# Optimization experiments

Hardware: AMD Instinct MI355X
Metric: run time of the kernel (lower is better)

The kernel has to match this reference:

```python
import jax, jax.numpy as jnp
import numpy as np

VOCAB = 50257
HIDDEN = 1024
CUTOFFS = [0, 20000, 40000, VOCAB]
N_CLUSTERS = 3
N_TOKENS = 4096


def setup_inputs() -> dict:
    key = jax.random.key(0)
    k1, k2, k3, k4 = jax.random.split(key, 4)
    x = jax.random.normal(k1, (N_TOKENS, HIDDEN), dtype=jnp.float32)
    y = jax.random.randint(k2, (N_TOKENS,), 0, VOCAB, dtype=jnp.int64)
    # nn.Linear(hidden, n_clusters, bias=False) weight: [n_clusters, hidden], init std=0.02
    W_cluster = jax.random.normal(k3, (N_CLUSTERS, HIDDEN), dtype=jnp.float32) * 0.02
    logits = jax.random.normal(k4, (HIDDEN, VOCAB), dtype=jnp.float32) * 0.02
    return {"x": x, "y": y, "W_cluster": W_cluster, "logits": logits}


def reference(x, y, W_cluster, logits):
    # cluster head: [N, n_clusters]
    cluster_ll = jax.nn.log_softmax(x @ W_cluster.T, axis=1)
    nll = jnp.zeros(y.shape, dtype=x.dtype)
    for i in range(N_CLUSTERS):  # small fixed loop over clusters
        l, r = CUTOFFS[i], CUTOFFS[i + 1]
        mask = (y >= l) & (y < r)
        # tail logits for this cluster's vocab slice: [N, r-l]
        tail_logprob = jax.nn.log_softmax(x @ logits[:, l:r], axis=1)
        t = jnp.clip(y - l, 0, r - l - 1)  # in-range for masked-out tokens
        tgt_lp = jnp.take_along_axis(tail_logprob, t[:, None], axis=1)[:, 0]
        val = -cluster_ll[:, i] - tgt_lp
        nll = jnp.where(mask, val, nll)
    return nll
```

## Files before the change

kernel.cpp:

```cpp
#include <hip/hip_runtime.h>
#include <math.h>

typedef unsigned short ushort_t;
typedef __attribute__((ext_vector_type(8))) short short8;
typedef __attribute__((ext_vector_type(4))) float floatx4;

constexpr int NT = 4096;
constexpr int H  = 1024;
constexpr int V  = 50257;
constexpr int CUT1 = 20000;
constexpr int CUT2 = 40000;

constexpr int NPAD_TOK = 4352;
constexpr int NPAD_COL = 50560;
constexpr int CT0 = 79, CT1 = 79, CT2 = 41;
constexpr int CT_TOTAL = CT0 + CT1 + CT2;
constexpr int MAX_TTILES = 16;
constexpr int CT_GROUPS = (CT_TOTAL + 7) / 8;
constexpr int MFMA_GRID = 8 * CT_GROUPS * MAX_TTILES;
constexpr int NKT = H / 32;

constexpr int FB_TILES0 = (20000 + 63) / 64;
constexpr int FB_TILES1 = (20000 + 63) / 64;
constexpr int FB_TILES2 = (V - 40000 + 63) / 64;
constexpr int FB_TOTAL = FB_TILES0 + FB_TILES1 + FB_TILES2;

__device__ __forceinline__ ushort_t f2bf(float f) {
  unsigned int u = __float_as_uint(f);
  u = (u + 0x7FFFu + ((u >> 16) & 1u)) >> 16;
  return (ushort_t)u;
}
__device__ __forceinline__ float bf2f(ushort_t b) {
  return __uint_as_float(((unsigned int)b) << 16);
}
__device__ __forceinline__ void gl_lds16(const void* g, void* l) {
  __builtin_amdgcn_global_load_lds(
      (const __attribute__((address_space(1))) void*)g,
      (__attribute__((address_space(3))) void*)l, 16, 0, 0);
}

__global__ __launch_bounds__(1024) void setup_kernel(
    const int* __restrict__ y, int* __restrict__ offsets,
    int* __restrict__ perm, float* __restrict__ sumexp) {
  __shared__ int wcnt[16][3];
  __shared__ int wstart[16][3];
  int tid = threadIdx.x, lane = tid & 63, wid = tid >> 6;
  for (int i = tid; i < NT; i += 1024) sumexp[i] = 0.f;

  int kc[4];
  unsigned long long msk[4][3];
  int cw0 = 0, cw1 = 0, cw2 = 0;
  #pragma unroll
  for (int e = 0; e < 4; e++) {
    int v = y[tid + e * 1024];
    kc[e] = (v >= CUT1) + (v >= CUT2);
    msk[e][0] = __ballot(kc[e] == 0);
    msk[e][1] = __ballot(kc[e] == 1);
    msk[e][2] = __ballot(kc[e] == 2);
    cw0 += __popcll(msk[e][0]);
    cw1 += __popcll(msk[e][1]);
    cw2 += __popcll(msk[e][2]);
  }
  if (lane == 0) { wcnt[wid][0] = cw0; wcnt[wid][1] = cw1; wcnt[wid][2] = cw2; }
  __syncthreads();
  if (tid == 0) {
    int t0 = 0, t1 = 0, t2 = 0;
    for (int wv = 0; wv < 16; wv++) { t0 += wcnt[wv][0]; t1 += wcnt[wv][1]; t2 += wcnt[wv][2]; }
    offsets[0] = 0; offsets[1] = t0; offsets[2] = t0 + t1; offsets[3] = NT;
    int c0 = 0, c1 = t0, c2 = t0 + t1;
    for (int wv = 0; wv < 16; wv++) {
      wstart[wv][0] = c0; c0 += wcnt[wv][0];
      wstart[wv][1] = c1; c1 += wcnt[wv][1];
      wstart[wv][2] = c2; c2 += wcnt[wv][2];
    }
  }
  __syncthreads();
  int r0 = wstart[wid][0], r1 = wstart[wid][1], r2 = wstart[wid][2];
  unsigned long long below = (1ull << lane) - 1ull;
  #pragma unroll
  for (int e = 0; e < 4; e++) {
    int t = tid + e * 1024;
    int c = kc[e];
    int start = (c == 0) ? r0 : ((c == 1) ? r1 : r2);
    perm[start + __popcll(msk[e][c] & below)] = t;
    r0 += __popcll(msk[e][0]);
    r1 += __popcll(msk[e][1]);
    r2 += __popcll(msk[e][2]);
  }
}

__global__ __launch_bounds__(256) void gather_kernel(
    const float* __restrict__ x, const int* __restrict__ perm,
    ushort_t* __restrict__ xb) {
  int p = blockIdx.x;
  int src = (p < NT) ? perm[p] : -1;
  int k = threadIdx.x * 4;
  ushort4 o;
  if (src >= 0) {
    float4 v = *(const float4*)&x[(size_t)src * H + k];
    o.x = f2bf(v.x); o.y = f2bf(v.y); o.z = f2bf(v.z); o.w = f2bf(v.w);
  } else {
    o.x = 0; o.y = 0; o.z = 0; o.w = 0;
  }
  *(ushort4*)&xb[(size_t)p * H + k] = o;
}

__global__ __launch_bounds__(256) void transpose_kernel(
    const float* __restrict__ logits, ushort_t* __restrict__ lt) {
  __shared__ float ts[64][129];
  int col0 = blockIdx.x * 128, k0 = blockIdx.y * 64;
  int tid = threadIdx.x;
  #pragma unroll
  for (int e = 0; e < 8; e++) {
    int i = e * 256 + tid;
    int r = i >> 5, q = i & 31;
    int col = col0 + q * 4;
    float4 v;
    if (col + 3 < V) {
      v = *(const float4*)&logits[(size_t)(k0 + r) * V + col];
    } else {
      v.x = (col + 0 < V) ? logits[(size_t)(k0 + r) * V + col + 0] : 0.f;
      v.y = (col + 1 < V) ? logits[(size_t)(k0 + r) * V + col + 1] : 0.f;
      v.z = (col + 2 < V) ? logits[(size_t)(k0 + r) * V + col + 2] : 0.f;
      v.w = (col + 3 < V) ? logits[(size_t)(k0 + r) * V + col + 3] : 0.f;
    }
    ts[r][4 * q + 0] = v.x;
    ts[r][4 * q + 1] = v.y;
    ts[r][4 * q + 2] = v.z;
    ts[r][4 * q + 3] = v.w;
  }
  __syncthreads();
  #pragma unroll
  for (int e = 0; e < 4; e++) {
    int i = e * 256 + tid;
    int col = i >> 3, kq8 = i & 7;
    short8 o;
    #pragma unroll
    for (int d = 0; d < 8; d++) o[d] = (short)f2bf(ts[8 * kq8 + d][col]);
    *(short8*)&lt[(size_t)(col0 + col) * H + k0 + 8 * kq8] = o;
  }
}

__global__ __launch_bounds__(256) void head_kernel(
    const float* __restrict__ x, const int* __restrict__ y,
    const float* __restrict__ Wc, const ushort_t* __restrict__ lt,
    float* __restrict__ neg_cll, float* __restrict__ z_tgt) {
  int tid = threadIdx.x;
  int lane = tid & 63;
  int token = blockIdx.x * 4 + (tid >> 6);
  int yv = y[token];
  const float* xp = x + (size_t)token * H;
  const ushort_t* lp = lt + (size_t)yv * H;
  float c0 = 0.f, c1 = 0.f, c2 = 0.f, zt = 0.f;
  #pragma unroll
  for (int j = 0; j < 16; j++) {
    int h = lane + j * 64;
    float xv = xp[h];
    c0 = fmaf(xv, Wc[h], c0);
    c1 = fmaf(xv, Wc[H + h], c1);
    c2 = fmaf(xv, Wc[2 * H + h], c2);
    zt = fmaf(xv, bf2f(lp[h]), zt);
  }
  #pragma unroll
  for (int d = 32; d; d >>= 1) {
    c0 += __shfl_down(c0, d);
    c1 += __shfl_down(c1, d);
    c2 += __shfl_down(c2, d);
    zt += __shfl_down(zt, d);
  }
  if (lane == 0) {
    float m = fmaxf(c0, fmaxf(c1, c2));
    float lse = m + logf(expf(c0 - m) + expf(c1 - m) + expf(c2 - m));
    int k = (yv >= CUT1) + (yv >= CUT2);
    float ck = (k == 0) ? c0 : ((k == 1) ? c1 : c2);
    neg_cll[token] = lse - ck;
    z_tgt[token] = zt;
  }
}

__global__ __launch_bounds__(512, 2) void mfma_kernel(
    const ushort_t* __restrict__ xb, const ushort_t* __restrict__ lt,
    const int* __restrict__ offsets, float* __restrict__ sumexp) {
  int id = blockIdx.x;
  int xcd = id & 7;
  int j = id >> 3;
  int ct = xcd + 8 * (j >> 4);
  int tt = j & 15;
  if (ct >= CT_TOTAL) return;

  int c, col0, colEnd;
  if (ct < CT0)            { c = 0; col0 = ct * 256;                      colEnd = CUT1; }
  else if (ct < CT0 + CT1) { c = 1; col0 = CUT1 + (ct - CT0) * 256;       colEnd = CUT2; }
  else                     { c = 2; col0 = CUT2 + (ct - CT0 - CT1) * 256; colEnd = V; }

  int t0 = offsets[c] + tt * 256;
  int tEnd = offsets[c + 1];
  if (t0 >= tEnd) return;

  __shared__ __align__(16) ushort_t As[4][128 * 64];
  __shared__ __align__(16) ushort_t Bs[4][128 * 64];

  int tid = threadIdx.x;
  int lane = tid & 63;
  int w = tid >> 6;
  int wm = w >> 2, wn = w & 3;
  int m_in = lane & 15, quad = lane >> 4;

  const ushort_t* gA[2];
  const ushort_t* gB[2];
  #pragma unroll
  for (int cc = 0; cc < 2; cc++) {
    int lr = w * 16 + cc * 8 + (lane >> 3);
    int ls = lane & 7;
    int m  = 2 * lr + (ls >> 2);
    int q  = (ls & 3) ^ (lr & 3);
    gA[cc] = xb + (size_t)(t0 + m) * H + q * 8;
    gB[cc] = lt + (size_t)(col0 + m) * H + q * 8;
  }
  int ks = 0;
  auto STAGE = [&]() {
    int b = ks & 3;
    #pragma unroll
    for (int cc = 0; cc < 2; cc++) {
      gl_lds16(gA[cc], &As[b][(w * 16 + cc * 8) * 64]);
      gl_lds16(gB[cc], &Bs[b][(w * 16 + cc * 8) * 64]);
      gA[cc] += 32; gB[cc] += 32;
    }
    ++ks;
  };

  int sxor = quad ^ ((m_in >> 1) & 3);
  int aoff = (wm * 64 + (m_in >> 1)) * 64 + (m_in & 1) * 32 + sxor * 8;
  int boff = (wn * 32 + (m_in >> 1)) * 64 + (m_in & 1) * 32 + sxor * 8;

  floatx4 acc[8][4];
  #pragma unroll
  for (int i = 0; i < 8; i++)
    #pragma unroll
    for (int jj = 0; jj < 4; jj++)
      acc[i][jj] = (floatx4){0.f, 0.f, 0.f, 0.f};

  STAGE(); STAGE(); STAGE();
  asm volatile("s_waitcnt vmcnt(8)" ::: "memory");
  __builtin_amdgcn_sched_barrier(0);
  __builtin_amdgcn_s_barrier();
  __builtin_amdgcn_sched_barrier(0);

  #pragma unroll 4
  for (int k = 0; k < NKT; ++k) {
    int b = k & 3;
    const ushort_t* Ab = &As[b][0];
    const ushort_t* Bb = &Bs[b][0];

    if (k + 3 < NKT) STAGE();
    __builtin_amdgcn_sched_barrier(0);

    short8 af[4], bf[4];
    #pragma unroll
    for (int i = 0; i < 4; i++) af[i] = *(const short8*)&Ab[aoff + i * 512];
    #pragma unroll
    for (int jj = 0; jj < 4; jj++) bf[jj] = *(const short8*)&Bb[boff + jj * 512];

    __builtin_amdgcn_s_setprio(1);
    #pragma unroll
    for (int i = 0; i < 4; i++)
      #pragma unroll
      for (int jj = 0; jj < 4; jj++)
        acc[i][jj] = __builtin_amdgcn_mfma_f32_16x16x32_bf16(af[i], bf[jj], acc[i][jj], 0, 0, 0);
    __builtin_amdgcn_s_setprio(0);

    #pragma unroll
    for (int i = 0; i < 4; i++) af[i] = *(const short8*)&Ab[aoff + (i + 4) * 512];

    __builtin_amdgcn_s_setprio(1);
    #pragma unroll
    for (int i = 0; i < 4; i++)
      #pragma unroll
      for (int jj = 0; jj < 4; jj++)
        acc[i + 4][jj] = __builtin_amdgcn_mfma_f32_16x16x32_bf16(af[i], bf[jj], acc[i + 4][jj], 0, 0, 0);
    __builtin_amdgcn_s_setprio(0);

    if (k < NKT - 1) {
      if (k < NKT - 3) {
        asm volatile("s_waitcnt vmcnt(8)" ::: "memory");
      } else if (k == NKT - 3) {
        asm volatile("s_waitcnt vmcnt(4)" ::: "memory");
      } else {
        asm volatile("s_waitcnt vmcnt(0)" ::: "memory");
      }
      __builtin_amdgcn_sched_barrier(0);
      __builtin_amdgcn_s_barrier();
      __builtin_amdgcn_sched_barrier(0);
    }
  }

  float* red = (float*)&As[0][0];
  #pragma unroll
  for (int i = 0; i < 8; i++) {
    #pragma unroll
    for (int r = 0; r < 4; r++) {
      float s = 0.f;
      #pragma unroll
      for (int jj = 0; jj < 4; jj++) {
        int col = col0 + wn * 64 + jj * 16 + m_in;
        if (col < colEnd) s += __expf(acc[i][jj][r]);
      }
      s += __shfl_down(s, 8, 16);
      s += __shfl_down(s, 4, 16);
      s += __shfl_down(s, 2, 16);
      s += __shfl_down(s, 1, 16);
      if (m_in == 0) red[w * 128 + i * 16 + quad * 4 + r] = s;
    }
  }
  __syncthreads();
  if (tid < 256) {
    int row = tid, wm2 = row >> 7, rw = row & 127;
    float s = red[(wm2 * 4 + 0) * 128 + rw] + red[(wm2 * 4 + 1) * 128 + rw] +
              red[(wm2 * 4 + 2) * 128 + rw] + red[(wm2 * 4 + 3) * 128 + rw];
    if (t0 + row < tEnd) atomicAdd(&sumexp[t0 + row], s);
  }
}

__global__ __launch_bounds__(256) void final_kernel(
    const int* __restrict__ perm, const float* __restrict__ neg_cll,
    const float* __restrict__ z_tgt, const float* __restrict__ sumexp,
    float* __restrict__ out) {
  int p = blockIdx.x * 256 + threadIdx.x;
  if (p < NT) {
    int t = perm[p];
    out[t] = neg_cll[t] + logf(sumexp[p]) - z_tgt[t];
  }
}

__global__ __launch_bounds__(256) void head_kernel_fb(
    const float* __restrict__ x, const int* __restrict__ y,
    const float* __restrict__ Wc, const float* __restrict__ logits,
    float* __restrict__ neg_cll, float* __restrict__ z_tgt) {
  int tid = threadIdx.x;
  int lane = tid & 63;
  int token = blockIdx.x * 4 + (tid >> 6);
  int yv = y[token];
  const float* xp = x + (size_t)token * H;
  float c0 = 0.f, c1 = 0.f, c2 = 0.f, zt = 0.f;
  #pragma unroll
  for (int j = 0; j < 16; j++) {
    int h = lane + j * 64;
    float xv = xp[h];
    c0 = fmaf(xv, Wc[h], c0);
    c1 = fmaf(xv, Wc[H + h], c1);
    c2 = fmaf(xv, Wc[2 * H + h], c2);
    zt = fmaf(xv, logits[(size_t)h * V + yv], zt);
  }
  #pragma unroll
  for (int d = 32; d; d >>= 1) {
    c0 += __shfl_down(c0, d);
    c1 += __shfl_down(c1, d);
    c2 += __shfl_down(c2, d);
    zt += __shfl_down(zt, d);
  }
  if (lane == 0) {
    float m = fmaxf(c0, fmaxf(c1, c2));
    float lse = m + logf(expf(c0 - m) + expf(c1 - m) + expf(c2 - m));
    int k = (yv >= CUT1) + (yv >= CUT2);
    float ck = (k == 0) ? c0 : ((k == 1) ? c1 : c2);
    neg_cll[token] = lse - ck;
    z_tgt[token] = zt;
  }
}

__global__ __launch_bounds__(256) void main_kernel_fb(
    const float* __restrict__ x, const float* __restrict__ logits,
    const int* __restrict__ offsets, const int* __restrict__ perm,
    float* __restrict__ sumexp) {
  int ct = blockIdx.x;
  int c, lct;
  if (ct < FB_TILES0)                  { c = 0; lct = ct; }
  else if (ct < FB_TILES0 + FB_TILES1) { c = 1; lct = ct - FB_TILES0; }
  else                                 { c = 2; lct = ct - FB_TILES0 - FB_TILES1; }
  int colBase = (c == 0) ? 0 : ((c == 1) ? CUT1 : CUT2);
  int colEnd  = (c == 0) ? CUT1 : ((c == 1) ? CUT2 : V);
  int col0 = colBase + lct * 64;
  int ncols = min(64, colEnd - col0);

  int t0 = offsets[c] + blockIdx.y * 64;
  int tEnd = offsets[c + 1];
  if (t0 >= tEnd) return;
  int ntok = min(64, tEnd - t0);

  __shared__ int tok_s[64];
  __shared__ float xsf[32][68];
  __shared__ float lsm[32][68];

  int tid = threadIdx.x;
  if (tid < 64) tok_s[tid] = perm[t0 + min(tid, ntok - 1)];
  __syncthreads();

  int tg = tid >> 4;
  int cg = tid & 15;
  float acc[4][4] = {};

  for (int h0 = 0; h0 < H; h0 += 32) {
    __syncthreads();
    #pragma unroll
    for (int e = 0; e < 8; e++) {
      int elem = e * 256 + tid;
      int tt = elem >> 5, kk = elem & 31;
      xsf[kk][tt] = x[(size_t)tok_s[tt] * H + h0 + kk];
    }
    #pragma unroll
    for (int e = 0; e < 8; e++) {
      int elem = e * 256 + tid;
      int kk = elem >> 6, cc = elem & 63;
      lsm[kk][cc] = (cc < ncols) ? logits[(size_t)(h0 + kk) * V + col0 + cc] : 0.f;
    }
    __syncthreads();
    #pragma unroll
    for (int kk = 0; kk < 32; kk++) {
      float4 xv = *(const float4*)&xsf[kk][4 * tg];
      float4 lv = *(const float4*)&lsm[kk][4 * cg];
      acc[0][0] = fmaf(xv.x, lv.x, acc[0][0]);
      acc[0][1] = fmaf(xv.x, lv.y, acc[0][1]);
      acc[0][2] = fmaf(xv.x, lv.z, acc[0][2]);
      acc[0][3] = fmaf(xv.x, lv.w, acc[0][3]);
      acc[1][0] = fmaf(xv.y, lv.x, acc[1][0]);
      acc[1][1] = fmaf(xv.y, lv.y, acc[1][1]);
      acc[1][2] = fmaf(xv.y, lv.z, acc[1][2]);
      acc[1][3] = fmaf(xv.y, lv.w, acc[1][3]);
      acc[2][0] = fmaf(xv.z, lv.x, acc[2][0]);
      acc[2][1] = fmaf(xv.z, lv.y, acc[2][1]);
      acc[2][2] = fmaf(xv.z, lv.z, acc[2][2]);
      acc[2][3] = fmaf(xv.z, lv.w, acc[2][3]);
      acc[3][0] = fmaf(xv.w, lv.x, acc[3][0]);
      acc[3][1] = fmaf(xv.w, lv.y, acc[3][1]);
      acc[3][2] = fmaf(xv.w, lv.z, acc[3][2]);
      acc[3][3] = fmaf(xv.w, lv.w, acc[3][3]);
    }
  }

  float s[4];
  #pragma unroll
  for (int i = 0; i < 4; i++) {
    float v = 0.f;
    #pragma unroll
    for (int j = 0; j < 4; j++) {
      if (4 * cg + j < ncols) v += expf(acc[i][j]);
    }
    s[i] = v;
  }
  #pragma unroll
  for (int i = 0; i < 4; i++) {
    #pragma unroll
    for (int d = 8; d; d >>= 1) s[i] += __shfl_down(s[i], d, 16);
  }
  if (cg == 0) {
    #pragma unroll
    for (int i = 0; i < 4; i++) {
      int tt = 4 * tg + i;
      if (tt < ntok) atomicAdd(&sumexp[tok_s[tt]], s[i]);
    }
  }
}

__global__ __launch_bounds__(256) void final_kernel_fb(
    const float* __restrict__ neg_cll, const float* __restrict__ z_tgt,
    const float* __restrict__ sumexp, float* __restrict__ out) {
  int i = blockIdx.x * 256 + threadIdx.x;
  if (i < NT) out[i] = neg_cll[i] + logf(sumexp[i]) - z_tgt[i];
}

extern "C" void kernel_launch(void* const* d_in, const int* in_sizes, int n_in,
                              void* d_out, int out_size, void* d_ws,
                              size_t ws_size, hipStream_t stream) {
  const float* x      = (const float*)d_in[0];
  const int*   y      = (const int*)d_in[1];
  const float* Wc     = (const float*)d_in[2];
  const float* logits = (const float*)d_in[3];
  float* out = (float*)d_out;

  char* ws = (char*)d_ws;
  int*   offsets = (int*)ws;
  int*   perm    = (int*)(ws + 256);
  float* sumexp  = (float*)(ws + 16896);
  float* neg_cll = (float*)(ws + 33280);
  float* z_tgt   = (float*)(ws + 49664);
  ushort_t* xb   = (ushort_t*)(ws + 66048);
  ushort_t* lt   = (ushort_t*)(ws + 66048 + (size_t)NPAD_TOK * H * 2);
  const size_t WS_NEED = 66048 + (size_t)NPAD_TOK * H * 2 + (size_t)NPAD_COL * H * 2;

  setup_kernel<<<1, 1024, 0, stream>>>(y, offsets, perm, sumexp);

  if (ws_size >= WS_NEED) {
    gather_kernel<<<NPAD_TOK, 256, 0, stream>>>(x, perm, xb);
    dim3 tg(NPAD_COL / 128, H / 64);
    transpose_kernel<<<tg, 256, 0, stream>>>(logits, lt);
    head_kernel<<<NT / 4, 256, 0, stream>>>(x, y, Wc, lt, neg_cll, z_tgt);
    mfma_kernel<<<MFMA_GRID, 512, 0, stream>>>(xb, lt, offsets, sumexp);
    final_kernel<<<NT / 256, 256, 0, stream>>>(perm, neg_cll, z_tgt, sumexp, out);
  } else {
    head_kernel_fb<<<NT / 4, 256, 0, stream>>>(x, y, Wc, logits, neg_cll, z_tgt);
    dim3 grid(FB_TOTAL, 64);
    main_kernel_fb<<<grid, 256, 0, stream>>>(x, logits, offsets, perm, sumexp);
    final_kernel_fb<<<NT / 256, 256, 0, stream>>>(neg_cll, z_tgt, sumexp, out);
  }
}
```

Baseline: 582.8 us.

## Restructure MFMA main loop into 64-wide K steps with 4-phase interleaved staging

Replaces the 4-deep ring of 32-wide K buffers with a double-buffered 64-wide K pipeline. Each iteration is split into four phases that interleave LDS fragment loads, global-to-LDS staging of the next A and B halves, and MFMA bursts, separated by barriers. The LDS swizzle changes to an 8-way XOR over full 128-byte rows. The aim is to halve loop iterations and overlap global loads with compute more finely, at the cost of more barriers per iteration and trickier vmcnt/lgkmcnt accounting.

```diff
diff --git a/kernel.cpp b/kernel.cpp
--- a/kernel.cpp
+++ b/kernel.cpp
@@ -18,7 +18,7 @@
 constexpr int MAX_TTILES = 16;
 constexpr int CT_GROUPS = (CT_TOTAL + 7) / 8;
 constexpr int MFMA_GRID = 8 * CT_GROUPS * MAX_TTILES;
-constexpr int NKT = H / 32;
+constexpr int NKT = H / 64;
 
 constexpr int FB_TILES0 = (20000 + 63) / 64;
 constexpr int FB_TILES1 = (20000 + 63) / 64;
@@ -188,17 +188,17 @@
   int tt = j & 15;
   if (ct >= CT_TOTAL) return;
 
-  int c, col0, colEnd;
-  if (ct < CT0)            { c = 0; col0 = ct * 256;                      colEnd = CUT1; }
-  else if (ct < CT0 + CT1) { c = 1; col0 = CUT1 + (ct - CT0) * 256;       colEnd = CUT2; }
-  else                     { c = 2; col0 = CUT2 + (ct - CT0 - CT1) * 256; colEnd = V; }
-
-  int t0 = offsets[c] + tt * 256;
-  int tEnd = offsets[c + 1];
+  int c_cl, col0, colEnd;
+  if (ct < CT0)            { c_cl = 0; col0 = ct * 256;                      colEnd = CUT1; }
+  else if (ct < CT0 + CT1) { c_cl = 1; col0 = CUT1 + (ct - CT0) * 256;       colEnd = CUT2; }
+  else                     { c_cl = 2; col0 = CUT2 + (ct - CT0 - CT1) * 256; colEnd = V; }
+
+  int t0 = offsets[c_cl] + tt * 256;
+  int tEnd = offsets[c_cl + 1];
   if (t0 >= tEnd) return;
 
-  __shared__ __align__(16) ushort_t As[4][128 * 64];
-  __shared__ __align__(16) ushort_t Bs[4][128 * 64];
+  __shared__ __align__(16) ushort_t As[2][256 * 64];
+  __shared__ __align__(16) ushort_t Bs[2][256 * 64];
 
   int tid = threadIdx.x;
   int lane = tid & 63;
@@ -206,32 +206,32 @@
   int wm = w >> 2, wn = w & 3;
   int m_in = lane & 15, quad = lane >> 4;
 
-  const ushort_t* gA[2];
-  const ushort_t* gB[2];
+  int qsw  = (lane & 7) ^ (lane >> 3);
+  int rofs = lane >> 3;
+  const ushort_t* pA[2];
+  const ushort_t* pB[2];
   #pragma unroll
   for (int cc = 0; cc < 2; cc++) {
-    int lr = w * 16 + cc * 8 + (lane >> 3);
-    int ls = lane & 7;
-    int m  = 2 * lr + (ls >> 2);
-    int q  = (ls & 3) ^ (lr & 3);
-    gA[cc] = xb + (size_t)(t0 + m) * H + q * 8;
-    gB[cc] = lt + (size_t)(col0 + m) * H + q * 8;
-  }
-  int ks = 0;
-  auto STAGE = [&]() {
-    int b = ks & 3;
-    #pragma unroll
-    for (int cc = 0; cc < 2; cc++) {
-      gl_lds16(gA[cc], &As[b][(w * 16 + cc * 8) * 64]);
-      gl_lds16(gB[cc], &Bs[b][(w * 16 + cc * 8) * 64]);
-      gA[cc] += 32; gB[cc] += 32;
-    }
-    ++ks;
+    pA[cc] = xb + (size_t)(t0 + w * 16 + cc * 8 + rofs) * H + qsw * 8;
+    pB[cc] = lt + (size_t)(col0 + w * 16 + cc * 8 + rofs) * H + qsw * 8;
+  }
+  auto STAGE_A = [&](int cA, int hi) {
+    #pragma unroll
+    for (int cc = 0; cc < 2; cc++)
+      gl_lds16(pA[cc] + (size_t)hi * 128 * H,
+               &As[cA][(hi * 128 + w * 16 + cc * 8) * 64]);
   };
-
-  int sxor = quad ^ ((m_in >> 1) & 3);
-  int aoff = (wm * 64 + (m_in >> 1)) * 64 + (m_in & 1) * 32 + sxor * 8;
-  int boff = (wn * 32 + (m_in >> 1)) * 64 + (m_in & 1) * 32 + sxor * 8;
+  auto STAGE_B = [&](int cB, int hi) {
+    #pragma unroll
+    for (int cc = 0; cc < 2; cc++)
+      gl_lds16(pB[cc] + (size_t)hi * 128 * H,
+               &Bs[cB][(hi * 128 + w * 16 + cc * 8) * 64]);
+  };
+
+  int sx0 = quad ^ (m_in & 7);
+  int sx1 = (4 + quad) ^ (m_in & 7);
+  int rbaseA = wm * 128 + m_in;
+  int rbaseB = wn * 64 + m_in;
 
   floatx4 acc[8][4];
   #pragma unroll
@@ -240,60 +240,99 @@
     for (int jj = 0; jj < 4; jj++)
       acc[i][jj] = (floatx4){0.f, 0.f, 0.f, 0.f};
 
-  STAGE(); STAGE(); STAGE();
-  asm volatile("s_waitcnt vmcnt(8)" ::: "memory");
-  __builtin_amdgcn_sched_barrier(0);
-  __builtin_amdgcn_s_barrier();
-  __builtin_amdgcn_sched_barrier(0);
-
-  #pragma unroll 4
-  for (int k = 0; k < NKT; ++k) {
-    int b = k & 3;
-    const ushort_t* Ab = &As[b][0];
-    const ushort_t* Bb = &Bs[b][0];
-
-    if (k + 3 < NKT) STAGE();
+  short8 af[2][2];
+  short8 bfr[4][2];
+
+#define LDA_PHASE(Q)                                                          \
+  do {                                                                        \
+    _Pragma("unroll") for (int ii = 0; ii < 2; ii++) {                        \
+      af[ii][0] = *(const short8*)&Ac[(rbaseA + (Q)*32 + ii*16)*64 + sx0*8];  \
+      af[ii][1] = *(const short8*)&Ac[(rbaseA + (Q)*32 + ii*16)*64 + sx1*8];  \
+    }                                                                         \
+  } while (0)
+
+#define MM_PHASE(Q)                                                           \
+  do {                                                                        \
+    __builtin_amdgcn_s_setprio(1);                                            \
+    _Pragma("unroll") for (int ii = 0; ii < 2; ii++)                          \
+      _Pragma("unroll") for (int jj = 0; jj < 4; jj++) {                      \
+        acc[2*(Q)+ii][jj] = __builtin_amdgcn_mfma_f32_16x16x32_bf16(          \
+            af[ii][0], bfr[jj][0], acc[2*(Q)+ii][jj], 0, 0, 0);               \
+        acc[2*(Q)+ii][jj] = __builtin_amdgcn_mfma_f32_16x16x32_bf16(          \
+            af[ii][1], bfr[jj][1], acc[2*(Q)+ii][jj], 0, 0, 0);               \
+      }                                                                       \
+    __builtin_amdgcn_s_setprio(0);                                            \
+  } while (0)
+
+#define WAIT_LGKM0                                                            \
+  asm volatile("s_waitcnt lgkmcnt(0)" ::: "memory");                          \
+  __builtin_amdgcn_sched_barrier(0)
+
+#define BAR                                                                   \
+  __builtin_amdgcn_sched_barrier(0);                                          \
+  __builtin_amdgcn_s_barrier();                                               \
+  __builtin_amdgcn_sched_barrier(0)
+
+  STAGE_B(0, 0); STAGE_B(0, 1); pB[0] += 64; pB[1] += 64;
+  STAGE_A(0, 0); STAGE_A(0, 1); pA[0] += 64; pA[1] += 64;
+  STAGE_B(1, 0); STAGE_B(1, 1); pB[0] += 64; pB[1] += 64;
+  asm volatile("s_waitcnt vmcnt(4)" ::: "memory");
+  BAR;
+
+  #pragma unroll 2
+  for (int n = 0; n < NKT; ++n) {
+    int c = n & 1;
+    const ushort_t* Ac = &As[c][0];
+    const ushort_t* Bc = &Bs[c][0];
+    bool stA = (n + 1 < NKT);
+    bool stB = (n + 2 < NKT);
+
+    #pragma unroll
+    for (int jj = 0; jj < 4; jj++) {
+      bfr[jj][0] = *(const short8*)&Bc[(rbaseB + jj * 16) * 64 + sx0 * 8];
+      bfr[jj][1] = *(const short8*)&Bc[(rbaseB + jj * 16) * 64 + sx1 * 8];
+    }
+    LDA_PHASE(0);
+    if (stA) STAGE_A(c ^ 1, 0);
+    asm volatile("s_waitcnt lgkmcnt(8)" ::: "memory");
+    BAR;
+    WAIT_LGKM0;
+    MM_PHASE(0);
+    BAR;
+
+    LDA_PHASE(1);
+    if (stA) { STAGE_A(c ^ 1, 1); pA[0] += 64; pA[1] += 64; }
+    BAR;
+    WAIT_LGKM0;
+    MM_PHASE(1);
+    BAR;
+
+    LDA_PHASE(2);
+    if (stB) STAGE_B(c, 0);
+    BAR;
+    WAIT_LGKM0;
+    MM_PHASE(2);
+    BAR;
+
+    LDA_PHASE(3);
+    if (stB) { STAGE_B(c, 1); pB[0] += 64; pB[1] += 64; }
+    BAR;
+    WAIT_LGKM0;
+    MM_PHASE(3);
     __builtin_amdgcn_sched_barrier(0);
-
-    short8 af[4], bf[4];
-    #pragma unroll
-    for (int i = 0; i < 4; i++) af[i] = *(const short8*)&Ab[aoff + i * 512];
-    #pragma unroll
-    for (int jj = 0; jj < 4; jj++) bf[jj] = *(const short8*)&Bb[boff + jj * 512];
-
-    __builtin_amdgcn_s_setprio(1);
-    #pragma unroll
-    for (int i = 0; i < 4; i++)
-      #pragma unroll
-      for (int jj = 0; jj < 4; jj++)
-        acc[i][jj] = __builtin_amdgcn_mfma_f32_16x16x32_bf16(af[i], bf[jj], acc[i][jj], 0, 0, 0);
-    __builtin_amdgcn_s_setprio(0);
-
-    #pragma unroll
-    for (int i = 0; i < 4; i++) af[i] = *(const short8*)&Ab[aoff + (i + 4) * 512];
-
-    __builtin_amdgcn_s_setprio(1);
-    #pragma unroll
-    for (int i = 0; i < 4; i++)
-      #pragma unroll
-      for (int jj = 0; jj < 4; jj++)
-        acc[i + 4][jj] = __builtin_amdgcn_mfma_f32_16x16x32_bf16(af[i], bf[jj], acc[i + 4][jj], 0, 0, 0);
-    __builtin_amdgcn_s_setprio(0);
-
-    if (k < NKT - 1) {
-      if (k < NKT - 3) {
-        asm volatile("s_waitcnt vmcnt(8)" ::: "memory");
-      } else if (k == NKT - 3) {
-        asm volatile("s_waitcnt vmcnt(4)" ::: "memory");
-      } else {
-        asm volatile("s_waitcnt vmcnt(0)" ::: "memory");
-      }
-      __builtin_amdgcn_sched_barrier(0);
-      __builtin_amdgcn_s_barrier();
-      __builtin_amdgcn_sched_barrier(0);
-    }
-  }
-
+    if (n < NKT - 2) {
+      asm volatile("s_waitcnt vmcnt(4)" ::: "memory");
+    } else if (n == NKT - 2) {
+      asm volatile("s_waitcnt vmcnt(0)" ::: "memory");
+    }
+    BAR;
+  }
+#undef LDA_PHASE
+#undef MM_PHASE
+#undef WAIT_LGKM0
+#undef BAR
+
+  __syncthreads();
   float* red = (float*)&As[0][0];
   #pragma unroll
   for (int i = 0; i < 8; i++) {
```

After: 524.2 us. -10.0%, faster.
